# Kernel tuning notes

Hardware: AMD Instinct MI355X
Metric: run time of the kernel (lower is better)

Reference implementation:

```python
import jax, jax.numpy as jnp
import numpy as np

N_FEATURES = 16384
N_EXPERTS = 8
D_IN = 768
EXPERT_DIM = N_FEATURES // N_EXPERTS  # 2048
N_TOKENS = 16384


def setup_inputs() -> dict:
    key = jax.random.key(0)
    k_act, k_preb, k_enc, k_dec, k_rb, k_r = jax.random.split(key, 6)
    activations = jax.random.normal(k_act, (N_TOKENS, D_IN), dtype=jnp.float32)
    pre_b = jax.random.normal(k_preb, (D_IN,), dtype=jnp.float32) * 0.01
    enc = jax.random.normal(k_enc, (N_EXPERTS, D_IN, EXPERT_DIM), dtype=jnp.float32) / (2.0 ** 0.5) / (D_IN ** 0.5)
    dec = jax.random.normal(k_dec, (N_EXPERTS, EXPERT_DIM, D_IN), dtype=jnp.float32) / (EXPERT_DIM ** 0.5)
    router_b = jax.random.normal(k_rb, (D_IN,), dtype=jnp.float32) * 0.01
    router = jax.random.normal(k_r, (D_IN, N_EXPERTS), dtype=jnp.float32) / (D_IN ** 0.5)
    return {"activations": activations, "pre_b": pre_b, "enc": enc, "dec": dec,
            "router_b": router_b, "router": router}


def reference(activations, pre_b, enc, dec, router_b, router):
    # Router: softmax over experts, top-1 routing.
    logits = (activations - router_b) @ router            # [N, E]
    probs = jax.nn.softmax(logits, axis=-1)
    expert_max_prob = jnp.max(probs, axis=-1)              # [N]
    expert_idx = jnp.argmax(probs, axis=-1)                # [N] int

    n_experts = enc.shape[0]
    recons = jnp.zeros_like(activations)
    # Fixed small loop over experts; tokens are masked (zeroed) per expert so
    # each per-expert encode/decode GEMM only contributes for its routed rows.
    for e in range(n_experts):
        mask = (expert_idx == e)[:, None]                  # [N, 1]
        x_e = jnp.where(mask, activations, 0.0)            # masked gather
        latent = jax.nn.relu(x_e @ enc[e])                 # [N, expert_dim]
        recon = latent @ dec[e]                            # [N, d_in]
        recons = recons + jnp.where(mask, recon, 0.0)      # scatter-combine

    return expert_max_prob[:, None] * recons + pre_b
```

## Files before the change

kernel.cpp:

```cpp
#include <hip/hip_runtime.h>
#include <hip/hip_bf16.h>
#include <hip/hip_fp16.h>

#define N_TOKENS 16384
#define D_IN 768
#define N_EXPERTS 8
#define EXPERT_DIM 2048

#define ROUTER_BLOCKS 256
#define TOK_PER_BLOCK 64

typedef _Float16 half8 __attribute__((ext_vector_type(8)));
typedef float floatx4 __attribute__((ext_vector_type(4)));

#define BM 128
#define BN 128
#define BK 32
#define NBUF 3

#define WAIT_VM8 0xF78
#define WAIT_VM4 0xF74
#define WAIT_VM0 0xF70

__device__ __forceinline__ void glds16(const _Float16* g, _Float16* l) {
    __builtin_amdgcn_global_load_lds(
        (const __attribute__((address_space(1))) unsigned int*)g,
        (__attribute__((address_space(3))) unsigned int*)l, 16, 0, 0);
}

__global__ __launch_bounds__(256) void convert_act(const float* __restrict__ act,
    _Float16* __restrict__ act_h)
{
    size_t i = ((size_t)blockIdx.x * 256 + threadIdx.x) * 8;
    float4 v0 = *(const float4*)(act + i);
    float4 v1 = *(const float4*)(act + i + 4);
    half8 h;
    h[0] = (_Float16)v0.x; h[1] = (_Float16)v0.y; h[2] = (_Float16)v0.z; h[3] = (_Float16)v0.w;
    h[4] = (_Float16)v1.x; h[5] = (_Float16)v1.y; h[6] = (_Float16)v1.z; h[7] = (_Float16)v1.w;
    *(half8*)(act_h + i) = h;
}

__global__ __launch_bounds__(256) void router_kernel(const float* __restrict__ act,
    const float* __restrict__ router_b, const float* __restrict__ router,
    float* __restrict__ prob, int* __restrict__ localpos, int* __restrict__ eidx,
    int* __restrict__ hist)
{
    __shared__ int h[N_EXPERTS];
    if (threadIdx.x < N_EXPERTS) h[threadIdx.x] = 0;
    __syncthreads();

    int wave = threadIdx.x >> 6, lane = threadIdx.x & 63;
#pragma unroll 1
    for (int it = 0; it < 16; ++it) {
        int t = blockIdx.x * TOK_PER_BLOCK + wave * 16 + it;
        float acc[8];
#pragma unroll
        for (int e = 0; e < 8; ++e) acc[e] = 0.f;
        const float* arow = act + (size_t)t * D_IN;
#pragma unroll
        for (int i0 = 0; i0 < D_IN; i0 += 64) {
            int i = i0 + lane;
            float a = arow[i] - router_b[i];
            const float* r = router + i * 8;
#pragma unroll
            for (int e = 0; e < 8; ++e) acc[e] += a * r[e];
        }
#pragma unroll
        for (int s = 32; s > 0; s >>= 1) {
#pragma unroll
            for (int e = 0; e < 8; ++e) acc[e] += __shfl_down(acc[e], s, 64);
        }
        if (lane == 0) {
            float m = acc[0]; int ai = 0;
#pragma unroll
            for (int e = 1; e < 8; ++e) if (acc[e] > m) { m = acc[e]; ai = e; }
            float s = 0.f;
#pragma unroll
            for (int e = 0; e < 8; ++e) s += __expf(acc[e] - m);
            prob[t] = 1.0f / s;
            eidx[t] = ai;
            localpos[t] = atomicAdd(&h[ai], 1);
        }
    }
    __syncthreads();
    if (threadIdx.x < N_EXPERTS) hist[blockIdx.x * N_EXPERTS + threadIdx.x] = h[threadIdx.x];
}

__global__ __launch_bounds__(256) void scan_kernel(int* __restrict__ hist,
    int* __restrict__ counts, int* __restrict__ offsets)
{
    __shared__ int sh[ROUTER_BLOCKS * N_EXPERTS];
    __shared__ int tot[N_EXPERTS], off[N_EXPERTS];
    int tid = threadIdx.x;
    *(int4*)&sh[tid * 8]     = *(const int4*)&hist[tid * 8];
    *(int4*)&sh[tid * 8 + 4] = *(const int4*)&hist[tid * 8 + 4];
    __syncthreads();
    if (tid < N_EXPERTS) {
        int run = 0;
        for (int b = 0; b < ROUTER_BLOCKS; ++b) {
            int v = sh[b * 8 + tid];
            sh[b * 8 + tid] = run;
            run += v;
        }
        tot[tid] = run;
    }
    __syncthreads();
    if (tid == 0) {
        int run = 0;
        for (int e = 0; e < N_EXPERTS; ++e) {
            off[e] = run; offsets[e] = run; counts[e] = tot[e]; run += tot[e];
        }
    }
    __syncthreads();
    int4 a = *(const int4*)&sh[tid * 8];
    int4 b = *(const int4*)&sh[tid * 8 + 4];
    a.x += off[0]; a.y += off[1]; a.z += off[2]; a.w += off[3];
    b.x += off[4]; b.y += off[5]; b.z += off[6]; b.w += off[7];
    *(int4*)&hist[tid * 8]     = a;
    *(int4*)&hist[tid * 8 + 4] = b;
}

__global__ __launch_bounds__(256) void order_kernel(const int* __restrict__ eidx,
    const int* __restrict__ localpos, const int* __restrict__ hist,
    int* __restrict__ order)
{
    int t = blockIdx.x * 256 + threadIdx.x;
    int base = hist[(t >> 6) * N_EXPERTS + eidx[t]];
    order[base + localpos[t]] = t;
}

__global__ __launch_bounds__(256) void transpose_to_half(const float* __restrict__ W,
    _Float16* __restrict__ WT, int K, int Nc)
{
    __shared__ _Float16 tile[64][72];
    size_t esz = (size_t)K * Nc;
    const float* We = W + (size_t)blockIdx.z * esz;
    _Float16* WTe = WT + (size_t)blockIdx.z * esz;
    int n0 = blockIdx.x * 64, k0 = blockIdx.y * 64;
    int tr = threadIdx.x >> 4;
    int tc = threadIdx.x & 15;
#pragma unroll
    for (int rr = 0; rr < 64; rr += 16) {
        int k = k0 + rr + tr;
        float4 v = *(const float4*)(We + (size_t)k * Nc + n0 + tc * 4);
        tile[tc * 4 + 0][rr + tr] = (_Float16)v.x;
        tile[tc * 4 + 1][rr + tr] = (_Float16)v.y;
        tile[tc * 4 + 2][rr + tr] = (_Float16)v.z;
        tile[tc * 4 + 3][rr + tr] = (_Float16)v.w;
    }
    __syncthreads();
#pragma unroll
    for (int p = 0; p < 2; ++p) {
        int id = threadIdx.x + p * 256;
        int r = id >> 3, ch = id & 7;
        half8 v = *(const half8*)&tile[r][ch * 8];
        *(half8*)(WTe + (size_t)(n0 + r) * K + k0 + ch * 8) = v;
    }
}

__global__ __launch_bounds__(256) void encode_kernel(const _Float16* __restrict__ act_h,
    const _Float16* __restrict__ encT, const int* __restrict__ order,
    const int* __restrict__ counts, const int* __restrict__ offsets,
    _Float16* __restrict__ latent)
{
    int id = blockIdx.x;
    int e = id & 7;
    int j = id >> 3;
    int nt = j & 15;
    int mt = j >> 4;

    int n_e = counts[e];
    if (mt * BM >= n_e) return;
    int slot0 = offsets[e] + mt * BM;
    int mrem = n_e - mt * BM;

    __shared__ _Float16 As[NBUF][BM * BK];
    __shared__ _Float16 Bs[NBUF][BN * BK];
    __shared__ int s_tok[BM];

    int tid = threadIdx.x;
    if (tid < BM) s_tok[tid] = (tid < mrem) ? order[slot0 + tid] : 0;
    __syncthreads();

    int wave = tid >> 6, lane = tid & 63;
    int wm = wave >> 1, wn = wave & 1;

    int r_lo = wave * 16 + (lane >> 2);
    int sc = lane & 3;
    int c = (sc - (r_lo >> 1)) & 3;
    const _Float16* Be = encT + (size_t)e * D_IN * EXPERT_DIM + (size_t)(nt * BN) * D_IN;
    const _Float16* pa0 = act_h + (size_t)s_tok[r_lo] * D_IN + c * 8;
    const _Float16* pa1 = act_h + (size_t)s_tok[r_lo + 64] * D_IN + c * 8;
    const _Float16* pb0 = Be + (size_t)r_lo * D_IN + c * 8;
    const _Float16* pb1 = Be + (size_t)(r_lo + 64) * D_IN + c * 8;

    int frag_off = ((((lane >> 4) + ((lane & 15) >> 1)) & 3) * 8);
    int mrow = lane & 15;

    floatx4 acc[4][4];
#pragma unroll
    for (int i = 0; i < 4; ++i)
#pragma unroll
        for (int j2 = 0; j2 < 4; ++j2) acc[i][j2] = (floatx4){0.f, 0.f, 0.f, 0.f};

#define ENC_ISSUE(kk, buf)                                            \
    do {                                                              \
        int k0_ = (kk) * BK;                                          \
        glds16(pa0 + k0_, &As[buf][(wave * 64) * 8]);                 \
        glds16(pa1 + k0_, &As[buf][(256 + wave * 64) * 8]);           \
        glds16(pb0 + k0_, &Bs[buf][(wave * 64) * 8]);                 \
        glds16(pb1 + k0_, &Bs[buf][(256 + wave * 64) * 8]);           \
    } while (0)

    const int NT = D_IN / BK;
    ENC_ISSUE(0, 0);
    ENC_ISSUE(1, 1);
    int buf = 0, nxt = 2;
#pragma unroll 1
    for (int k = 0; k < NT; ++k) {
        if (k + 2 < NT) {
            ENC_ISSUE(k + 2, nxt);
            __builtin_amdgcn_s_waitcnt(WAIT_VM8);
        } else if (k + 1 < NT) {
            __builtin_amdgcn_s_waitcnt(WAIT_VM4);
        } else {
            __builtin_amdgcn_s_waitcnt(WAIT_VM0);
        }
        __builtin_amdgcn_s_barrier();
        half8 af[4], bf[4];
#pragma unroll
        for (int i = 0; i < 4; ++i) af[i] = *(const half8*)&As[buf][(wm * 64 + i * 16 + mrow) * BK + frag_off];
#pragma unroll
        for (int i = 0; i < 4; ++i) bf[i] = *(const half8*)&Bs[buf][(wn * 64 + i * 16 + mrow) * BK + frag_off];
#pragma unroll
        for (int i = 0; i < 4; ++i)
#pragma unroll
            for (int j2 = 0; j2 < 4; ++j2)
                acc[i][j2] = __builtin_amdgcn_mfma_f32_16x16x32_f16(af[i], bf[j2], acc[i][j2], 0, 0, 0);
        __builtin_amdgcn_s_barrier();
        buf = (buf == NBUF - 1) ? 0 : buf + 1;
        nxt = (nxt == NBUF - 1) ? 0 : nxt + 1;
    }
#undef ENC_ISSUE

    int crow_base = wm * 64 + (lane >> 4) * 4;
    int ccol_base = nt * BN + wn * 64 + (lane & 15);
#pragma unroll
    for (int i = 0; i < 4; ++i) {
#pragma unroll
        for (int j2 = 0; j2 < 4; ++j2) {
#pragma unroll
            for (int r = 0; r < 4; ++r) {
                int row = crow_base + i * 16 + r;
                if (row < mrem) {
                    float v = acc[i][j2][r];
                    v = v > 0.f ? v : 0.f;
                    latent[(size_t)(slot0 + row) * EXPERT_DIM + ccol_base + j2 * 16] = (_Float16)v;
                }
            }
        }
    }
}

__global__ __launch_bounds__(256) void decode_kernel(const _Float16* __restrict__ latent,
    const _Float16* __restrict__ decT, const int* __restrict__ order,
    const int* __restrict__ counts, const int* __restrict__ offsets,
    const float* __restrict__ prob, const float* __restrict__ pre_b,
    float* __restrict__ out)
{
    int id = blockIdx.x;
    int e = id & 7;
    int j = id >> 3;
    int nt = j % 6;
    int mt = j / 6;

    int n_e = counts[e];
    if (mt * BM >= n_e) return;
    int slot0 = offsets[e] + mt * BM;
    int mrem = n_e - mt * BM;

    __shared__ _Float16 As[NBUF][BM * BK];
    __shared__ _Float16 Bs[NBUF][BN * BK];
    __shared__ int s_tok[BM];
    __shared__ float s_p[BM];

    int tid = threadIdx.x;
    if (tid < BM) {
        int tok = (tid < mrem) ? order[slot0 + tid] : 0;
        s_tok[tid] = tok;
        s_p[tid] = prob[tok];
    }
    __syncthreads();

    const _Float16* Ae = latent + (size_t)slot0 * EXPERT_DIM;
    const _Float16* Be = decT + (size_t)e * EXPERT_DIM * D_IN + (size_t)(nt * BN) * EXPERT_DIM;

    int wave = tid >> 6, lane = tid & 63;
    int wm = wave >> 1, wn = wave & 1;

    int r_lo = wave * 16 + (lane >> 2);
    int sc = lane & 3;
    int c = (sc - (r_lo >> 1)) & 3;
    const _Float16* pa0 = Ae + (size_t)r_lo * EXPERT_DIM + c * 8;
    const _Float16* pa1 = Ae + (size_t)(r_lo + 64) * EXPERT_DIM + c * 8;
    const _Float16* pb0 = Be + (size_t)r_lo * EXPERT_DIM + c * 8;
    const _Float16* pb1 = Be + (size_t)(r_lo + 64) * EXPERT_DIM + c * 8;

    int frag_off = ((((lane >> 4) + ((lane & 15) >> 1)) & 3) * 8);
    int mrow = lane & 15;

    floatx4 acc[4][4];
#pragma unroll
    for (int i = 0; i < 4; ++i)
#pragma unroll
        for (int j2 = 0; j2 < 4; ++j2) acc[i][j2] = (floatx4){0.f, 0.f, 0.f, 0.f};

#define DEC_ISSUE(kk, buf)                                            \
    do {                                                              \
        int k0_ = (kk) * BK;                                          \
        glds16(pa0 + k0_, &As[buf][(wave * 64) * 8]);                 \
        glds16(pa1 + k0_, &As[buf][(256 + wave * 64) * 8]);           \
        glds16(pb0 + k0_, &Bs[buf][(wave * 64) * 8]);                 \
        glds16(pb1 + k0_, &Bs[buf][(256 + wave * 64) * 8]);           \
    } while (0)

    const int NT = EXPERT_DIM / BK;
    DEC_ISSUE(0, 0);
    DEC_ISSUE(1, 1);
    int buf = 0, nxt = 2;
#pragma unroll 1
    for (int k = 0; k < NT; ++k) {
        if (k + 2 < NT) {
            DEC_ISSUE(k + 2, nxt);
            __builtin_amdgcn_s_waitcnt(WAIT_VM8);
        } else if (k + 1 < NT) {
            __builtin_amdgcn_s_waitcnt(WAIT_VM4);
        } else {
            __builtin_amdgcn_s_waitcnt(WAIT_VM0);
        }
        __builtin_amdgcn_s_barrier();
        half8 af[4], bf[4];
#pragma unroll
        for (int i = 0; i < 4; ++i) af[i] = *(const half8*)&As[buf][(wm * 64 + i * 16 + mrow) * BK + frag_off];
#pragma unroll
        for (int i = 0; i < 4; ++i) bf[i] = *(const half8*)&Bs[buf][(wn * 64 + i * 16 + mrow) * BK + frag_off];
#pragma unroll
        for (int i = 0; i < 4; ++i)
#pragma unroll
            for (int j2 = 0; j2 < 4; ++j2)
                acc[i][j2] = __builtin_amdgcn_mfma_f32_16x16x32_f16(af[i], bf[j2], acc[i][j2], 0, 0, 0);
        __builtin_amdgcn_s_barrier();
        buf = (buf == NBUF - 1) ? 0 : buf + 1;
        nxt = (nxt == NBUF - 1) ? 0 : nxt + 1;
    }
#undef DEC_ISSUE

    int crow_base = wm * 64 + (lane >> 4) * 4;
    int ccol_base = nt * BN + wn * 64 + (lane & 15);
#pragma unroll
    for (int i = 0; i < 4; ++i) {
#pragma unroll
        for (int j2 = 0; j2 < 4; ++j2) {
            int col = ccol_base + j2 * 16;
            float pb = pre_b[col];
#pragma unroll
            for (int r = 0; r < 4; ++r) {
                int row = crow_base + i * 16 + r;
                if (row < mrem) {
                    out[(size_t)s_tok[row] * D_IN + col] = s_p[row] * acc[i][j2][r] + pb;
                }
            }
        }
    }
}

extern "C" void kernel_launch(void* const* d_in, const int* in_sizes, int n_in,
                              void* d_out, int out_size, void* d_ws, size_t ws_size,
                              hipStream_t stream)
{
    const float* act      = (const float*)d_in[0];
    const float* pre_b    = (const float*)d_in[1];
    const float* enc      = (const float*)d_in[2];
    const float* dec      = (const float*)d_in[3];
    const float* router_b = (const float*)d_in[4];
    const float* router   = (const float*)d_in[5];
    float* out = (float*)d_out;

    char* w = (char*)d_ws;
    int* counts  = (int*)w;  w += 256;
    int* offsets = (int*)w;  w += 256;
    int* hist    = (int*)w;  w += ROUTER_BLOCKS * N_EXPERTS * 4;
    int* eidx    = (int*)w;  w += N_TOKENS * 4;
    int* lpos    = (int*)w;  w += N_TOKENS * 4;
    int* order   = (int*)w;  w += N_TOKENS * 4;
    float* prob  = (float*)w; w += N_TOKENS * 4;
    _Float16* act_h  = (_Float16*)w; w += (size_t)N_TOKENS * D_IN * 2;
    _Float16* encT   = (_Float16*)w; w += (size_t)N_EXPERTS * D_IN * EXPERT_DIM * 2;
    _Float16* decT   = (_Float16*)w; w += (size_t)N_EXPERTS * D_IN * EXPERT_DIM * 2;
    _Float16* latent = (_Float16*)w; w += (size_t)(N_TOKENS + BM) * EXPERT_DIM * 2;

    router_kernel<<<ROUTER_BLOCKS, 256, 0, stream>>>(act, router_b, router, prob, lpos, eidx, hist);
    scan_kernel<<<1, 256, 0, stream>>>(hist, counts, offsets);
    order_kernel<<<N_TOKENS / 256, 256, 0, stream>>>(eidx, lpos, hist, order);

    convert_act<<<N_TOKENS * D_IN / (256 * 8), 256, 0, stream>>>(act, act_h);
    transpose_to_half<<<dim3(EXPERT_DIM / 64, D_IN / 64, N_EXPERTS), 256, 0, stream>>>(enc, encT, D_IN, EXPERT_DIM);
    transpose_to_half<<<dim3(D_IN / 64, EXPERT_DIM / 64, N_EXPERTS), 256, 0, stream>>>(dec, decT, EXPERT_DIM, D_IN);

    encode_kernel<<<16384, 256, 0, stream>>>(act_h, encT, order, counts, offsets, latent);
    decode_kernel<<<6144, 256, 0, stream>>>(latent, decT, order, counts, offsets, prob, pre_b, out);
}
```

Before: 389.4 us.

## Enlarge grouped GEMM tiles to 256x256x64 with 8 waves and double buffering

Replaces the 128x128x32 triple-buffered encode and decode GEMMs with 256x256 tiles, BK=64, 512-thread blocks and a double-buffered LDS pipeline using an 8-way XOR-style swizzle. Each wave now computes a 128x64 sub-tile with 32 accumulators, raising arithmetic intensity and cutting how often the activation and weight tiles are reloaded. It also adds s_setprio around the MFMA bursts. The larger tiles waste more work on partial expert tiles, use 128KB of LDS, and need more registers, which can lower occupancy.

```diff
diff --git a/kernel.cpp b/kernel.cpp
--- a/kernel.cpp
+++ b/kernel.cpp
@@ -13,13 +13,10 @@
 typedef _Float16 half8 __attribute__((ext_vector_type(8)));
 typedef float floatx4 __attribute__((ext_vector_type(4)));
 
-#define BM 128
-#define BN 128
-#define BK 32
-#define NBUF 3
-
-#define WAIT_VM8 0xF78
-#define WAIT_VM4 0xF74
+#define GBM 256
+#define GBN 256
+#define GBK 64
+
 #define WAIT_VM0 0xF70
 
 __device__ __forceinline__ void glds16(const _Float16* g, _Float16* l) {
@@ -158,7 +155,19 @@
     }
 }
 
-__global__ __launch_bounds__(256) void encode_kernel(const _Float16* __restrict__ act_h,
+#define STAGE8(bufp, k0h)                                              \
+    do {                                                               \
+        glds16(pa0 + (k0h), (bufp) + 0 * 4096 + st_dst);               \
+        glds16(pa1 + (k0h), (bufp) + 1 * 4096 + st_dst);               \
+        glds16(pa2 + (k0h), (bufp) + 2 * 4096 + st_dst);               \
+        glds16(pa3 + (k0h), (bufp) + 3 * 4096 + st_dst);               \
+        glds16(pb0 + (k0h), (bufp) + 16384 + 0 * 4096 + st_dst);       \
+        glds16(pb1 + (k0h), (bufp) + 16384 + 1 * 4096 + st_dst);       \
+        glds16(pb2 + (k0h), (bufp) + 16384 + 2 * 4096 + st_dst);       \
+        glds16(pb3 + (k0h), (bufp) + 16384 + 3 * 4096 + st_dst);       \
+    } while (0)
+
+__global__ __launch_bounds__(512, 2) void encode_kernel(const _Float16* __restrict__ act_h,
     const _Float16* __restrict__ encT, const int* __restrict__ order,
     const int* __restrict__ counts, const int* __restrict__ offsets,
     _Float16* __restrict__ latent)
@@ -166,103 +175,113 @@
     int id = blockIdx.x;
     int e = id & 7;
     int j = id >> 3;
-    int nt = j & 15;
-    int mt = j >> 4;
+    int nt = j & 7;
+    int mt = j >> 3;
 
     int n_e = counts[e];
-    if (mt * BM >= n_e) return;
-    int slot0 = offsets[e] + mt * BM;
-    int mrem = n_e - mt * BM;
-
-    __shared__ _Float16 As[NBUF][BM * BK];
-    __shared__ _Float16 Bs[NBUF][BN * BK];
-    __shared__ int s_tok[BM];
+    if (mt * GBM >= n_e) return;
+    int slot0 = offsets[e] + mt * GBM;
+    int mrem = n_e - mt * GBM;
+
+    __shared__ _Float16 lds[2][32768];
+    __shared__ int s_tok[GBM];
 
     int tid = threadIdx.x;
-    if (tid < BM) s_tok[tid] = (tid < mrem) ? order[slot0 + tid] : 0;
-    __syncthreads();
-
-    int wave = tid >> 6, lane = tid & 63;
-    int wm = wave >> 1, wn = wave & 1;
-
-    int r_lo = wave * 16 + (lane >> 2);
-    int sc = lane & 3;
-    int c = (sc - (r_lo >> 1)) & 3;
-    const _Float16* Be = encT + (size_t)e * D_IN * EXPERT_DIM + (size_t)(nt * BN) * D_IN;
-    const _Float16* pa0 = act_h + (size_t)s_tok[r_lo] * D_IN + c * 8;
-    const _Float16* pa1 = act_h + (size_t)s_tok[r_lo + 64] * D_IN + c * 8;
-    const _Float16* pb0 = Be + (size_t)r_lo * D_IN + c * 8;
-    const _Float16* pb1 = Be + (size_t)(r_lo + 64) * D_IN + c * 8;
-
-    int frag_off = ((((lane >> 4) + ((lane & 15) >> 1)) & 3) * 8);
+    if (tid < GBM) s_tok[tid] = (tid < mrem) ? order[slot0 + tid] : order[slot0];
+    __syncthreads();
+
+    int w = tid >> 6, lane = tid & 63;
+    int wm = w >> 2, wn = w & 3;
     int mrow = lane & 15;
 
-    floatx4 acc[4][4];
-#pragma unroll
-    for (int i = 0; i < 4; ++i)
-#pragma unroll
-        for (int j2 = 0; j2 < 4; ++j2) acc[i][j2] = (floatx4){0.f, 0.f, 0.f, 0.f};
-
-#define ENC_ISSUE(kk, buf)                                            \
-    do {                                                              \
-        int k0_ = (kk) * BK;                                          \
-        glds16(pa0 + k0_, &As[buf][(wave * 64) * 8]);                 \
-        glds16(pa1 + k0_, &As[buf][(256 + wave * 64) * 8]);           \
-        glds16(pb0 + k0_, &Bs[buf][(wave * 64) * 8]);                 \
-        glds16(pb1 + k0_, &Bs[buf][(256 + wave * 64) * 8]);           \
-    } while (0)
-
-    const int NT = D_IN / BK;
-    ENC_ISSUE(0, 0);
-    ENC_ISSUE(1, 1);
-    int buf = 0, nxt = 2;
+    int st_dst = w * 512 + lane * 8;
+    int c_st = ((lane & 7) - (w << 2) - (lane >> 4)) & 7;
+    int row_st = w * 8 + (lane >> 3);
+    const _Float16* Be = encT + (size_t)e * D_IN * EXPERT_DIM + (size_t)(nt * GBN) * D_IN;
+    const _Float16* pa0 = act_h + (size_t)s_tok[0 * 64 + row_st] * D_IN + c_st * 8;
+    const _Float16* pa1 = act_h + (size_t)s_tok[1 * 64 + row_st] * D_IN + c_st * 8;
+    const _Float16* pa2 = act_h + (size_t)s_tok[2 * 64 + row_st] * D_IN + c_st * 8;
+    const _Float16* pa3 = act_h + (size_t)s_tok[3 * 64 + row_st] * D_IN + c_st * 8;
+    const _Float16* pb0 = Be + (size_t)(0 * 64 + row_st) * D_IN + c_st * 8;
+    const _Float16* pb1 = Be + (size_t)(1 * 64 + row_st) * D_IN + c_st * 8;
+    const _Float16* pb2 = Be + (size_t)(2 * 64 + row_st) * D_IN + c_st * 8;
+    const _Float16* pb3 = Be + (size_t)(3 * 64 + row_st) * D_IN + c_st * 8;
+
+    int c0 = ((lane >> 4) + (mrow >> 1)) & 7;
+    int aoff0 = (wm * 128 + mrow) * 64 + c0 * 8;
+    int aoff1 = (wm * 128 + mrow) * 64 + (c0 ^ 4) * 8;
+    int boff0 = 16384 + (wn * 64 + mrow) * 64 + c0 * 8;
+    int boff1 = 16384 + (wn * 64 + mrow) * 64 + (c0 ^ 4) * 8;
+
+    floatx4 acc[8][4];
+#pragma unroll
+    for (int i = 0; i < 8; ++i)
+#pragma unroll
+        for (int jj = 0; jj < 4; ++jj) acc[i][jj] = (floatx4){0.f, 0.f, 0.f, 0.f};
+
+    const int T = D_IN / GBK;
+    STAGE8(&lds[0][0], 0);
+    __builtin_amdgcn_s_waitcnt(WAIT_VM0);
+    __builtin_amdgcn_s_barrier();
+
 #pragma unroll 1
-    for (int k = 0; k < NT; ++k) {
-        if (k + 2 < NT) {
-            ENC_ISSUE(k + 2, nxt);
-            __builtin_amdgcn_s_waitcnt(WAIT_VM8);
-        } else if (k + 1 < NT) {
-            __builtin_amdgcn_s_waitcnt(WAIT_VM4);
-        } else {
+    for (int t = 0; t < T; ++t) {
+        _Float16* cur = &lds[t & 1][0];
+        if (t + 1 < T) {
+            _Float16* nxt = &lds[(t + 1) & 1][0];
+            int k1 = (t + 1) * GBK;
+            STAGE8(nxt, k1);
+        }
+        half8 a0[8], b0[4];
+#pragma unroll
+        for (int i = 0; i < 8; ++i) a0[i] = *(const half8*)&cur[aoff0 + i * 1024];
+#pragma unroll
+        for (int jj = 0; jj < 4; ++jj) b0[jj] = *(const half8*)&cur[boff0 + jj * 1024];
+        __builtin_amdgcn_s_setprio(1);
+#pragma unroll
+        for (int i = 0; i < 8; ++i)
+#pragma unroll
+            for (int jj = 0; jj < 4; ++jj)
+                acc[i][jj] = __builtin_amdgcn_mfma_f32_16x16x32_f16(a0[i], b0[jj], acc[i][jj], 0, 0, 0);
+        __builtin_amdgcn_s_setprio(0);
+        half8 a1[8], b1[4];
+#pragma unroll
+        for (int i = 0; i < 8; ++i) a1[i] = *(const half8*)&cur[aoff1 + i * 1024];
+#pragma unroll
+        for (int jj = 0; jj < 4; ++jj) b1[jj] = *(const half8*)&cur[boff1 + jj * 1024];
+        __builtin_amdgcn_s_setprio(1);
+#pragma unroll
+        for (int i = 0; i < 8; ++i)
+#pragma unroll
+            for (int jj = 0; jj < 4; ++jj)
+                acc[i][jj] = __builtin_amdgcn_mfma_f32_16x16x32_f16(a1[i], b1[jj], acc[i][jj], 0, 0, 0);
+        __builtin_amdgcn_s_setprio(0);
+        if (t + 1 < T) {
             __builtin_amdgcn_s_waitcnt(WAIT_VM0);
-        }
-        __builtin_amdgcn_s_barrier();
-        half8 af[4], bf[4];
-#pragma unroll
-        for (int i = 0; i < 4; ++i) af[i] = *(const half8*)&As[buf][(wm * 64 + i * 16 + mrow) * BK + frag_off];
-#pragma unroll
-        for (int i = 0; i < 4; ++i) bf[i] = *(const half8*)&Bs[buf][(wn * 64 + i * 16 + mrow) * BK + frag_off];
-#pragma unroll
-        for (int i = 0; i < 4; ++i)
-#pragma unroll
-            for (int j2 = 0; j2 < 4; ++j2)
-                acc[i][j2] = __builtin_amdgcn_mfma_f32_16x16x32_f16(af[i], bf[j2], acc[i][j2], 0, 0, 0);
-        __builtin_amdgcn_s_barrier();
-        buf = (buf == NBUF - 1) ? 0 : buf + 1;
-        nxt = (nxt == NBUF - 1) ? 0 : nxt + 1;
-    }
-#undef ENC_ISSUE
-
-    int crow_base = wm * 64 + (lane >> 4) * 4;
-    int ccol_base = nt * BN + wn * 64 + (lane & 15);
-#pragma unroll
-    for (int i = 0; i < 4; ++i) {
-#pragma unroll
-        for (int j2 = 0; j2 < 4; ++j2) {
+            __builtin_amdgcn_s_barrier();
+        }
+    }
+
+#pragma unroll
+    for (int i = 0; i < 8; ++i) {
+        int row0 = wm * 128 + i * 16 + (lane >> 4) * 4;
+#pragma unroll
+        for (int jj = 0; jj < 4; ++jj) {
+            int col = nt * GBN + wn * 64 + jj * 16 + mrow;
 #pragma unroll
             for (int r = 0; r < 4; ++r) {
-                int row = crow_base + i * 16 + r;
+                int row = row0 + r;
                 if (row < mrem) {
-                    float v = acc[i][j2][r];
+                    float v = acc[i][jj][r];
                     v = v > 0.f ? v : 0.f;
-                    latent[(size_t)(slot0 + row) * EXPERT_DIM + ccol_base + j2 * 16] = (_Float16)v;
+                    latent[(size_t)(slot0 + row) * EXPERT_DIM + col] = (_Float16)v;
                 }
             }
         }
     }
 }
 
-__global__ __launch_bounds__(256) void decode_kernel(const _Float16* __restrict__ latent,
+__global__ __launch_bounds__(512, 2) void decode_kernel(const _Float16* __restrict__ latent,
     const _Float16* __restrict__ decT, const int* __restrict__ order,
     const int* __restrict__ counts, const int* __restrict__ offsets,
     const float* __restrict__ prob, const float* __restrict__ pre_b,
@@ -271,103 +290,111 @@
     int id = blockIdx.x;
     int e = id & 7;
     int j = id >> 3;
-    int nt = j % 6;
-    int mt = j / 6;
+    int nt = j % 3;
+    int mt = j / 3;
 
     int n_e = counts[e];
-    if (mt * BM >= n_e) return;
-    int slot0 = offsets[e] + mt * BM;
-    int mrem = n_e - mt * BM;
-
-    __shared__ _Float16 As[NBUF][BM * BK];
-    __shared__ _Float16 Bs[NBUF][BN * BK];
-    __shared__ int s_tok[BM];
-    __shared__ float s_p[BM];
+    if (mt * GBM >= n_e) return;
+    int slot0 = offsets[e] + mt * GBM;
+    int mrem = n_e - mt * GBM;
+
+    __shared__ _Float16 lds[2][32768];
+    __shared__ int s_tok[GBM];
+    __shared__ float s_p[GBM];
 
     int tid = threadIdx.x;
-    if (tid < BM) {
-        int tok = (tid < mrem) ? order[slot0 + tid] : 0;
+    if (tid < GBM) {
+        int tok = (tid < mrem) ? order[slot0 + tid] : order[slot0];
         s_tok[tid] = tok;
         s_p[tid] = prob[tok];
     }
     __syncthreads();
 
+    int w = tid >> 6, lane = tid & 63;
+    int wm = w >> 2, wn = w & 3;
+    int mrow = lane & 15;
+
+    int st_dst = w * 512 + lane * 8;
+    int c_st = ((lane & 7) - (w << 2) - (lane >> 4)) & 7;
+    int row_st = w * 8 + (lane >> 3);
     const _Float16* Ae = latent + (size_t)slot0 * EXPERT_DIM;
-    const _Float16* Be = decT + (size_t)e * EXPERT_DIM * D_IN + (size_t)(nt * BN) * EXPERT_DIM;
-
-    int wave = tid >> 6, lane = tid & 63;
-    int wm = wave >> 1, wn = wave & 1;
-
-    int r_lo = wave * 16 + (lane >> 2);
-    int sc = lane & 3;
-    int c = (sc - (r_lo >> 1)) & 3;
-    const _Float16* pa0 = Ae + (size_t)r_lo * EXPERT_DIM + c * 8;
-    const _Float16* pa1 = Ae + (size_t)(r_lo + 64) * EXPERT_DIM + c * 8;
-    const _Float16* pb0 = Be + (size_t)r_lo * EXPERT_DIM + c * 8;
-    const _Float16* pb1 = Be + (size_t)(r_lo + 64) * EXPERT_DIM + c * 8;
-
-    int frag_off = ((((lane >> 4) + ((lane & 15) >> 1)) & 3) * 8);
-    int mrow = lane & 15;
-
-    floatx4 acc[4][4];
-#pragma unroll
-    for (int i = 0; i < 4; ++i)
-#pragma unroll
-        for (int j2 = 0; j2 < 4; ++j2) acc[i][j2] = (floatx4){0.f, 0.f, 0.f, 0.f};
-
-#define DEC_ISSUE(kk, buf)                                            \
-    do {                                                              \
-        int k0_ = (kk) * BK;                                          \
-        glds16(pa0 + k0_, &As[buf][(wave * 64) * 8]);                 \
-        glds16(pa1 + k0_, &As[buf][(256 + wave * 64) * 8]);           \
-        glds16(pb0 + k0_, &Bs[buf][(wave * 64) * 8]);                 \
-        glds16(pb1 + k0_, &Bs[buf][(256 + wave * 64) * 8]);           \
-    } while (0)
-
-    const int NT = EXPERT_DIM / BK;
-    DEC_ISSUE(0, 0);
-    DEC_ISSUE(1, 1);
-    int buf = 0, nxt = 2;
+    const _Float16* Be = decT + (size_t)e * EXPERT_DIM * D_IN + (size_t)(nt * GBN) * EXPERT_DIM;
+    const _Float16* pa0 = Ae + (size_t)(0 * 64 + row_st) * EXPERT_DIM + c_st * 8;
+    const _Float16* pa1 = Ae + (size_t)(1 * 64 + row_st) * EXPERT_DIM + c_st * 8;
+    const _Float16* pa2 = Ae + (size_t)(2 * 64 + row_st) * EXPERT_DIM + c_st * 8;
+    const _Float16* pa3 = Ae + (size_t)(3 * 64 + row_st) * EXPERT_DIM + c_st * 8;
+    const _Float16* pb0 = Be + (size_t)(0 * 64 + row_st) * EXPERT_DIM + c_st * 8;
+    const _Float16* pb1 = Be + (size_t)(1 * 64 + row_st) * EXPERT_DIM + c_st * 8;
+    const _Float16* pb2 = Be + (size_t)(2 * 64 + row_st) * EXPERT_DIM + c_st * 8;
+    const _Float16* pb3 = Be + (size_t)(3 * 64 + row_st) * EXPERT_DIM + c_st * 8;
+
+    int c0 = ((lane >> 4) + (mrow >> 1)) & 7;
+    int aoff0 = (wm * 128 + mrow) * 64 + c0 * 8;
+    int aoff1 = (wm * 128 + mrow) * 64 + (c0 ^ 4) * 8;
+    int boff0 = 16384 + (wn * 64 + mrow) * 64 + c0 * 8;
+    int boff1 = 16384 + (wn * 64 + mrow) * 64 + (c0 ^ 4) * 8;
+
+    floatx4 acc[8][4];
+#pragma unroll
+    for (int i = 0; i < 8; ++i)
+#pragma unroll
+        for (int jj = 0; jj < 4; ++jj) acc[i][jj] = (floatx4){0.f, 0.f, 0.f, 0.f};
+
+    const int T = EXPERT_DIM / GBK;
+    STAGE8(&lds[0][0], 0);
+    __builtin_amdgcn_s_waitcnt(WAIT_VM0);
+    __builtin_amdgcn_s_barrier();
+
 #pragma unroll 1
-    for (int k = 0; k < NT; ++k) {
-        if (k + 2 < NT) {
-            DEC_ISSUE(k + 2, nxt);
-            __builtin_amdgcn_s_waitcnt(WAIT_VM8);
-        } else if (k + 1 < NT) {
-            __builtin_amdgcn_s_waitcnt(WAIT_VM4);
-        } else {
+    for (int t = 0; t < T; ++t) {
+        _Float16* cur = &lds[t & 1][0];
+        if (t + 1 < T) {
+            _Float16* nxt = &lds[(t + 1) & 1][0];
+            int k1 = (t + 1) * GBK;
+            STAGE8(nxt, k1);
+        }
+        half8 a0[8], b0[4];
+#pragma unroll
+        for (int i = 0; i < 8; ++i) a0[i] = *(const half8*)&cur[aoff0 + i * 1024];
+#pragma unroll
+        for (int jj = 0; jj < 4; ++jj) b0[jj] = *(const half8*)&cur[boff0 + jj * 1024];
+        __builtin_amdgcn_s_setprio(1);
+#pragma unroll
+        for (int i = 0; i < 8; ++i)
+#pragma unroll
+            for (int jj = 0; jj < 4; ++jj)
+                acc[i][jj] = __builtin_amdgcn_mfma_f32_16x16x32_f16(a0[i], b0[jj], acc[i][jj], 0, 0, 0);
+        __builtin_amdgcn_s_setprio(0);
+        half8 a1[8], b1[4];
+#pragma unroll
+        for (int i = 0; i < 8; ++i) a1[i] = *(const half8*)&cur[aoff1 + i * 1024];
+#pragma unroll
+        for (int jj = 0; jj < 4; ++jj) b1[jj] = *(const half8*)&cur[boff1 + jj * 1024];
+        __builtin_amdgcn_s_setprio(1);
+#pragma unroll
+        for (int i = 0; i < 8; ++i)
+#pragma unroll
+            for (int jj = 0; jj < 4; ++jj)
+                acc[i][jj] = __builtin_amdgcn_mfma_f32_16x16x32_f16(a1[i], b1[jj], acc[i][jj], 0, 0, 0);
+        __builtin_amdgcn_s_setprio(0);
+        if (t + 1 < T) {
             __builtin_amdgcn_s_waitcnt(WAIT_VM0);
-        }
-        __builtin_amdgcn_s_barrier();
-        half8 af[4], bf[4];
-#pragma unroll
-        for (int i = 0; i < 4; ++i) af[i] = *(const half8*)&As[buf][(wm * 64 + i * 16 + mrow) * BK + frag_off];
-#pragma unroll
-        for (int i = 0; i < 4; ++i) bf[i] = *(const half8*)&Bs[buf][(wn * 64 + i * 16 + mrow) * BK + frag_off];
-#pragma unroll
-        for (int i = 0; i < 4; ++i)
-#pragma unroll
-            for (int j2 = 0; j2 < 4; ++j2)
-                acc[i][j2] = __builtin_amdgcn_mfma_f32_16x16x32_f16(af[i], bf[j2], acc[i][j2], 0, 0, 0);
-        __builtin_amdgcn_s_barrier();
-        buf = (buf == NBUF - 1) ? 0 : buf + 1;
-        nxt = (nxt == NBUF - 1) ? 0 : nxt + 1;
-    }
-#undef DEC_ISSUE
-
-    int crow_base = wm * 64 + (lane >> 4) * 4;
-    int ccol_base = nt * BN + wn * 64 + (lane & 15);
-#pragma unroll
-    for (int i = 0; i < 4; ++i) {
-#pragma unroll
-        for (int j2 = 0; j2 < 4; ++j2) {
-            int col = ccol_base + j2 * 16;
+            __builtin_amdgcn_s_barrier();
+        }
+    }
+
+#pragma unroll
+    for (int i = 0; i < 8; ++i) {
+        int row0 = wm * 128 + i * 16 + (lane >> 4) * 4;
+#pragma unroll
+        for (int jj = 0; jj < 4; ++jj) {
+            int col = nt * GBN + wn * 64 + jj * 16 + mrow;
             float pb = pre_b[col];
 #pragma unroll
             for (int r = 0; r < 4; ++r) {
-                int row = crow_base + i * 16 + r;
+                int row = row0 + r;
                 if (row < mrem) {
-                    out[(size_t)s_tok[row] * D_IN + col] = s_p[row] * acc[i][j2][r] + pb;
+                    out[(size_t)s_tok[row] * D_IN + col] = s_p[row] * acc[i][jj][r] + pb;
                 }
             }
         }
@@ -397,7 +424,7 @@
     _Float16* act_h  = (_Float16*)w; w += (size_t)N_TOKENS * D_IN * 2;
     _Float16* encT   = (_Float16*)w; w += (size_t)N_EXPERTS * D_IN * EXPERT_DIM * 2;
     _Float16* decT   = (_Float16*)w; w += (size_t)N_EXPERTS * D_IN * EXPERT_DIM * 2;
-    _Float16* latent = (_Float16*)w; w += (size_t)(N_TOKENS + BM) * EXPERT_DIM * 2;
+    _Float16* latent = (_Float16*)w; w += (size_t)(N_TOKENS + GBM) * EXPERT_DIM * 2;
 
     router_kernel<<<ROUTER_BLOCKS, 256, 0, stream>>>(act, router_b, router, prob, lpos, eidx, hist);
     scan_kernel<<<1, 256, 0, stream>>>(hist, counts, offsets);
@@ -407,6 +434,6 @@
     transpose_to_half<<<dim3(EXPERT_DIM / 64, D_IN / 64, N_EXPERTS), 256, 0, stream>>>(enc, encT, D_IN, EXPERT_DIM);
     transpose_to_half<<<dim3(D_IN / 64, EXPERT_DIM / 64, N_EXPERTS), 256, 0, stream>>>(dec, decT, EXPERT_DIM, D_IN);
 
-    encode_kernel<<<16384, 256, 0, stream>>>(act_h, encT, order, counts, offsets, latent);
-    decode_kernel<<<6144, 256, 0, stream>>>(latent, decT, order, counts, offsets, prob, pre_b, out);
-}
+    encode_kernel<<<4096, 512, 0, stream>>>(act_h, encT, order, counts, offsets, latent);
+    decode_kernel<<<1536, 512, 0, stream>>>(latent, decT, order, counts, offsets, prob, pre_b, out);
+}
```

Result: no change. 385.0 us (-1.1%).
